# Performance work log

Hardware: AMD Instinct MI355X
Metric: run time of the kernel (lower is better)

Reference implementation:

```python
import jax, jax.numpy as jnp
import numpy as np
import math

H = 10  # hidden_dim (hardcoded in source)
D = 2   # data_dim (hardcoded in source)
T = 256
B = 2048

PARAM_SHAPES = {
    'fi_in_W': (D, H), 'fi_in_b': (H,), 'fi_h_W': (H, H), 'fi_h_b': (H,),
    'fi_mu_W': (H, H), 'fi_mu_b': (H,), 'fi_sg_W': (H, H), 'fi_sg_b': (H,),
    'inf_in_W': (D, H), 'inf_in_b': (H,), 'inf_j_W': (2 * H, H), 'inf_j_b': (H,),
    'inf_h_W': (H, H), 'inf_h_b': (H,), 'inf_mu_W': (H, H), 'inf_mu_b': (H,),
    'inf_sg_W': (H, H), 'inf_sg_b': (H,),
    'tr_h_W': (H, H), 'tr_h_b': (H,), 'tr_mu_W': (H, H), 'tr_mu_b': (H,),
    'tr_sg_W': (H, H), 'tr_sg_b': (H,),
    'gen_h1_W': (H, H), 'gen_h1_b': (H,), 'gen_h2_W': (H, H), 'gen_h2_b': (H,),
    'gen_mu_W': (H, D), 'gen_mu_b': (D,), 'gen_sg_W': (H, D), 'gen_sg_b': (D,),
}


def setup_inputs() -> dict:
    key = jax.random.key(0)
    names = list(PARAM_SHAPES)
    keys = jax.random.split(key, len(names) + 2)
    inp = {}
    inp['sequence'] = jax.random.normal(keys[0], (T, B, D), jnp.float32)
    inp['noise'] = jax.random.normal(keys[1], (T, B, H), jnp.float32)
    for n, k in zip(names, keys[2:]):
        inp[n] = 0.1 * jax.random.normal(k, PARAM_SHAPES[n], jnp.float32)
    # Transition sigma is tanh(.); shift its bias so sigma stays strictly positive
    # (a trained model would do the same; negative sigma makes the source's log(prod) NaN).
    inp['tr_sg_b'] = inp['tr_sg_b'] + 2.0
    return inp


def _forward(sequence, noise,
             fi_in_W, fi_in_b, fi_h_W, fi_h_b, fi_mu_W, fi_mu_b, fi_sg_W, fi_sg_b,
             inf_in_W, inf_in_b, inf_j_W, inf_j_b, inf_h_W, inf_h_b, inf_mu_W, inf_mu_b, inf_sg_W, inf_sg_b,
             tr_h_W, tr_h_b, tr_mu_W, tr_mu_b, tr_sg_W, tr_sg_b,
             gen_h1_W, gen_h1_b, gen_h2_W, gen_h2_b, gen_mu_W, gen_mu_b, gen_sg_W, gen_sg_b):

    def first_inf(x):
        h = jnp.tanh(x @ fi_in_W + fi_in_b)
        h = jnp.tanh(h @ fi_h_W + fi_h_b)
        return jnp.tanh(h @ fi_mu_W + fi_mu_b), jax.nn.sigmoid(h @ fi_sg_W + fi_sg_b) + 0.001

    def inference(x, z):
        e = jnp.tanh(x @ inf_in_W + inf_in_b)
        h = jnp.tanh(jnp.concatenate([e, z], -1) @ inf_j_W + inf_j_b)
        h = jnp.tanh(h @ inf_h_W + inf_h_b)
        return jnp.tanh(h @ inf_mu_W + inf_mu_b), jax.nn.sigmoid(h @ inf_sg_W + inf_sg_b) + 0.001

    def transition(z):
        h = jnp.tanh(z @ tr_h_W + tr_h_b)
        return jnp.tanh(h @ tr_mu_W + tr_mu_b), jnp.tanh(h @ tr_sg_W + tr_sg_b)

    def generator(z):
        h = jax.nn.relu(z @ gen_h1_W + gen_h1_b)
        h = jax.nn.relu(h @ gen_h2_W + gen_h2_b)
        return jax.nn.sigmoid(h @ gen_mu_W + gen_mu_b), jax.nn.sigmoid(h @ gen_sg_W + gen_sg_b)

    def kld(mu_q, sg_q, mu_p, sg_p):  # source GaussianKLD (treats sigma as variance)
        a = jnp.log(jnp.prod(sg_p, -1) / jnp.prod(sg_q, -1))
        b = jnp.sum(sg_q / sg_p, -1)
        c = jnp.sum((mu_p - mu_q) ** 2 / sg_p, -1)
        return 0.5 * (a + b + c - mu_q.shape[-1])

    def gll(mu, sg, target):  # source GaussianLL (note: log(pi), not 2*pi — faithful)
        a = jnp.log(jnp.prod(sg, -1))
        b = jnp.sum((target - mu) ** 2 / sg, -1)
        c = mu.shape[-1] * math.log(math.pi)
        return -0.5 * (a + b + c)

    # t = 0: first_inference against unit-Gaussian prior
    q_mu0, q_sg0 = first_inf(sequence[0])
    kl0 = kld(q_mu0, q_sg0, jnp.zeros_like(q_mu0), jnp.ones_like(q_sg0))
    z1 = q_mu0 + q_sg0 * noise[0]
    g_mu0, g_sg0 = generator(z1)
    loss0 = kl0 + gll(g_mu0, g_sg0, sequence[0])  # [B]

    def step(z_prev, xe):
        x_t, eps = xe
        pr_mu, pr_sg = transition(z_prev)
        q_mu, q_sg = inference(x_t, z_prev)
        kl_t = kld(q_mu, q_sg, pr_mu, pr_sg)
        z = q_mu + q_sg * eps
        m, s = generator(z)
        ll_t = gll(m, s, x_t)
        return z, (m, kl_t + ll_t)

    _, (gens_rest, step_losses) = jax.lax.scan(step, z1, (sequence[1:], noise[1:]))
    generations = jnp.concatenate([g_mu0[None], gens_rest], 0)  # [T, B, D]
    loss = loss0 + jnp.sum(step_losses, 0)                       # [B]
    return generations, -loss / sequence.shape[0]


def reference(sequence, noise,
              fi_in_W, fi_in_b, fi_h_W, fi_h_b, fi_mu_W, fi_mu_b, fi_sg_W, fi_sg_b,
              inf_in_W, inf_in_b, inf_j_W, inf_j_b, inf_h_W, inf_h_b, inf_mu_W, inf_mu_b, inf_sg_W, inf_sg_b,
              tr_h_W, tr_h_b, tr_mu_W, tr_mu_b, tr_sg_W, tr_sg_b,
              gen_h1_W, gen_h1_b, gen_h2_W, gen_h2_b, gen_mu_W, gen_mu_b, gen_sg_W, gen_sg_b):
    return _forward(sequence, noise,
                    fi_in_W, fi_in_b, fi_h_W, fi_h_b, fi_mu_W, fi_mu_b, fi_sg_W, fi_sg_b,
                    inf_in_W, inf_in_b, inf_j_W, inf_j_b, inf_h_W, inf_h_b, inf_mu_W, inf_mu_b, inf_sg_W, inf_sg_b,
                    tr_h_W, tr_h_b, tr_mu_W, tr_mu_b, tr_sg_W, tr_sg_b,
                    gen_h1_W, gen_h1_b, gen_h2_W, gen_h2_b, gen_mu_W, gen_mu_b, gen_sg_W, gen_sg_b)
```

## Files before the change

### kernel.cpp

```cpp
#include <hip/hip_runtime.h>
#include <math.h>

#define T_STEPS 256
#define BATCH   2048
#define HID     10

#define S2P  2.8853900817779268f
#define SNP -1.4426950408889634f
#define LN2  0.6931471805599453f
#define LOGPI 1.1447298858494002f

typedef float v2f __attribute__((ext_vector_type(2)));

__device__ __forceinline__ float frcp(float x){ return __builtin_amdgcn_rcpf(x); }
__device__ __forceinline__ float ex2 (float x){ return __builtin_amdgcn_exp2f(x); }
__device__ __forceinline__ float ftanh2(float y){ return 1.f - 2.f*frcp(1.f + ex2(y)); }
__device__ __forceinline__ float fsigm2(float y){ return frcp(1.f + ex2(y)); }

template<int K> __device__ __forceinline__ float rotk(float x){
  return __int_as_float(__builtin_amdgcn_update_dpp(
      0, __float_as_int(x), 0x120 + K, 0xF, 0xF, false));
}
#define ROT16(r, v) do{ float _v=(v); r[0]=_v; \
  r[1]=rotk<1>(_v);  r[2]=rotk<2>(_v);  r[3]=rotk<3>(_v);  r[4]=rotk<4>(_v);  \
  r[5]=rotk<5>(_v);  r[6]=rotk<6>(_v);  r[7]=rotk<7>(_v);  r[8]=rotk<8>(_v);  \
  r[9]=rotk<9>(_v);  r[10]=rotk<10>(_v);r[11]=rotk<11>(_v);r[12]=rotk<12>(_v);\
  r[13]=rotk<13>(_v);r[14]=rotk<14>(_v);r[15]=rotk<15>(_v); }while(0)

__device__ __forceinline__ float dot16(const float* r, const float* w, float bias){
  float a0 = fmaf(r[0], w[0], bias);
  float a1 = r[1]*w[1];
  float a2 = r[2]*w[2];
  float a3 = r[3]*w[3];
  #pragma unroll
  for (int k=4;k<16;k+=4){
    a0 = fmaf(r[k  ], w[k  ], a0);
    a1 = fmaf(r[k+1], w[k+1], a1);
    a2 = fmaf(r[k+2], w[k+2], a2);
    a3 = fmaf(r[k+3], w[k+3], a3);
  }
  return (a0+a1)+(a2+a3);
}
__device__ __forceinline__ v2f dotp16s(const float* r, const v2f* w, v2f init){
  v2f a0 = __builtin_elementwise_fma((v2f){r[0],r[0]}, w[0], init);
  v2f a1 = (v2f){r[1],r[1]}*w[1];
  v2f a2 = (v2f){r[2],r[2]}*w[2];
  v2f a3 = (v2f){r[3],r[3]}*w[3];
  #pragma unroll
  for (int k=4;k<16;k+=4){
    a0 = __builtin_elementwise_fma((v2f){r[k  ],r[k  ]}, w[k  ], a0);
    a1 = __builtin_elementwise_fma((v2f){r[k+1],r[k+1]}, w[k+1], a1);
    a2 = __builtin_elementwise_fma((v2f){r[k+2],r[k+2]}, w[k+2], a2);
    a3 = __builtin_elementwise_fma((v2f){r[k+3],r[k+3]}, w[k+3], a3);
  }
  return (a0+a1)+(a2+a3);
}

template<int NROW, int NCOL>
__device__ __forceinline__ void loadrot(float* dst, const float* W, int j, int col,
                                        bool colok, float scale){
  int colc = colok ? col : 0;
  #pragma unroll
  for (int k=0;k<16;k++){
    int i = (j - k) & 15;
    bool v = colok && (i < NROW);
    int ic = v ? i : 0;
    float w = W[ic*NCOL + colc];
    dst[k] = v ? scale*w : 0.f;
  }
}
__device__ __forceinline__ float bload(const float* p, int idx, bool ok, float scale){
  float t = p[ok ? idx : 0];
  return ok ? scale*t : 0.f;
}
template<int X> __device__ __forceinline__ float xor16(float x){
  return __int_as_float(__builtin_amdgcn_ds_swizzle(__float_as_int(x), (X<<10)|0x1f));
}

struct P34 { const float* p[34]; float* out; };

__global__ __attribute__((amdgpu_flat_work_group_size(128, 128), amdgpu_waves_per_eu(1, 1)))
void k_fused(P34 prm)
{
  __shared__ float s_ae[2][64];
  __shared__ float s_z [2][64];
  __shared__ float s_t0[4];

  const int tx   = threadIdx.x;
  const int wid  = tx >> 6;
  const int lane = tx & 63;
  const int j    = lane & 15;
  const int grp  = lane >> 4;
  const int b    = blockIdx.x*4 + grp;
  const bool act = (j < HID);
  const int  jl  = act ? j : 0;

  const float* __restrict__ seq   = prm.p[0];
  const float* __restrict__ noise = prm.p[1];
  float* __restrict__ out = prm.out;

  if (wid == 0){
    float w_jz[16]; loadrot<10,10>(w_jz, prm.p[12] + 100, j, j, act, S2P);
    float w_h [16]; loadrot<10,10>(w_h,  prm.p[14],       j, j, act, S2P);
    float tmu [16]; loadrot<10,10>(tmu,  prm.p[16],       j, j, act, S2P);
    float tsg [16]; loadrot<10,10>(tsg,  prm.p[18],       j, j, act, SNP);
    v2f wmsg[16];
    #pragma unroll
    for (int k=0;k<16;k++) wmsg[k] = (v2f){tmu[k], tsg[k]};
    float b_in_h  = bload(prm.p[15], jl, act, S2P);
    const v2f bmsg = (v2f){bload(prm.p[17], jl, act, S2P), bload(prm.p[19], jl, act, SNP)};
    float wth [16]; loadrot<10,10>(wth,  prm.p[20], j, j, act, S2P);
    float bth  = bload(prm.p[21], jl, act, S2P);
    float ttmu[16]; loadrot<10,10>(ttmu, prm.p[22], j, j, act, S2P);
    float ttsg[16]; loadrot<10,10>(ttsg, prm.p[24], j, j, act, S2P);
    v2f wpr[16];
    #pragma unroll
    for (int k=0;k<16;k++) wpr[k] = (v2f){ttmu[k], ttsg[k]};
    const v2f bpr = (v2f){bload(prm.p[23], jl, act, S2P), bload(prm.p[25], jl, act, S2P)};

    float LL = 0.f, L2 = 0.f;
    auto lde = [&](int t){ return noise[t*BATCH*HID + b*HID + jl]; };

    float z_prev;
    {
      float w0 = bload(prm.p[2],      jl, act, S2P);
      float w1 = bload(prm.p[2], 10 + jl, act, S2P);
      float bb = bload(prm.p[3], jl, act, S2P);
      float f_h[16], f_mu[16], f_sg[16];
      loadrot<10,10>(f_h,  prm.p[4], j, j, act, S2P);  float fb_h  = bload(prm.p[5], jl, act, S2P);
      loadrot<10,10>(f_mu, prm.p[6], j, j, act, S2P);  float fb_mu = bload(prm.p[7], jl, act, S2P);
      loadrot<10,10>(f_sg, prm.p[8], j, j, act, SNP);  float fb_sg = bload(prm.p[9], jl, act, SNP);
      float2 x0 = *reinterpret_cast<const float2*>(seq + b*2);
      float eps = lde(0);
      float h0 = ftanh2(fmaf(x0.x, w0, fmaf(x0.y, w1, bb)));
      float r0[16]; ROT16(r0, h0);
      float h1 = ftanh2(dot16(r0, f_h, fb_h));
      float r1[16]; ROT16(r1, h1);
      float mu = ftanh2(dot16(r1, f_mu, fb_mu));
      float sg = fsigm2(dot16(r1, f_sg, fb_sg)) + 0.001f;
      if (act){ LL += sg + mu*mu; L2 -= __log2f(sg); }
      z_prev = fmaf(sg, eps, mu);
      s_z[0][lane] = z_prev;
    }
    float e0=lde(1), e1=lde(2), e2=lde(3), e3=lde(4);
    __syncthreads();

    auto w0step = [&](const float* aeb, float* zb, float ec){
      float aev = aeb[lane];
      float rz[16]; ROT16(rz, z_prev);
      float hj = ftanh2(aev + dot16(rz, w_jz, 0.f));
      float rhj[16]; ROT16(rhj, hj);
      float hi = ftanh2(dot16(rhj, w_h, b_in_h));
      float rhi[16]; ROT16(rhi, hi);
      v2f d2 = dotp16s(rhi, wmsg, bmsg);
      float q_mu = ftanh2(d2.x);
      float q_sg = fsigm2(d2.y) + 0.001f;
      float z = fmaf(q_sg, ec, q_mu);
      zb[lane] = z;
      float th = ftanh2(dot16(rz, wth, bth));
      float rth[16]; ROT16(rth, th);
      v2f d3 = dotp16s(rth, wpr, bpr);
      float prmu = ftanh2(d3.x);
      float prsg = ftanh2(d3.y);
      if (act){
        float dmu = prmu - q_mu;
        float rp  = frcp(prsg);
        LL += (q_sg + dmu*dmu)*rp;
        L2 += __log2f(prsg) - __log2f(q_sg);
      }
      z_prev = z;
    };

    for (int p = 0; p < 125; ++p){
      int s = 2*p + 1;
      float n0 = lde(s+4), n1 = lde(s+5);
      w0step(s_ae[1], s_z[1], e0); __syncthreads();
      w0step(s_ae[0], s_z[0], e1); __syncthreads();
      e0=e2; e1=e3; e2=n0; e3=n1;
    }
    float e255 = lde(255);
    w0step(s_ae[1], s_z[1], e0);   __syncthreads();
    w0step(s_ae[0], s_z[0], e1);   __syncthreads();
    w0step(s_ae[1], s_z[1], e2);   __syncthreads();
    w0step(s_ae[0], s_z[0], e3);   __syncthreads();
    w0step(s_ae[1], s_z[1], e255); __syncthreads();

    float tot = fmaf(LN2, L2, LL);
    tot += xor16<1>(tot); tot += xor16<2>(tot); tot += xor16<4>(tot); tot += xor16<8>(tot);
    if (j == 0) s_t0[grp] = tot;
    __syncthreads();
  } else {
    float w_ii0   = bload(prm.p[10],      jl, act, S2P);
    float w_ii1   = bload(prm.p[10], 10 + jl, act, S2P);
    float b_in_in = bload(prm.p[11], jl, act, S2P);
    float w_je[16]; loadrot<10,10>(w_je, prm.p[12], j, j, act, S2P);
    float b_in_j  = bload(prm.p[13], jl, act, S2P);

    float wg1[16]; loadrot<10,10>(wg1, prm.p[26], j, j, act, 1.f);
    float bg1 = bload(prm.p[27], jl, act, 1.f);
    float wg2[16]; loadrot<10,10>(wg2, prm.p[28], j, j, act, 1.f);
    float bg2 = bload(prm.p[29], jl, act, 1.f);
    const bool isd = (j < 4);
    const float* Wgo = (j < 2) ? prm.p[30] : prm.p[32];
    const float* Bgo = (j < 2) ? prm.p[31] : prm.p[33];
    float wgo[16]; loadrot<10,2>(wgo, Wgo, j, j & 1, isd, SNP);
    float bgo = bload(Bgo, j & 1, isd, SNP);

    float LL = 0.f, L2 = 0.f;
    auto ldx = [&](int t){ return *reinterpret_cast<const float2*>(seq + t*BATCH*2 + b*2); };

    {
      float2 x1 = ldx(1);
      float e = ftanh2(fmaf(x1.x, w_ii0, fmaf(x1.y, w_ii1, b_in_in)));
      float re[16]; ROT16(re, e);
      s_ae[1][lane] = dot16(re, w_je, b_in_j);
    }
    float2 xA = ldx(0), xB = ldx(1), xC = ldx(2), xD = ldx(3);
    __syncthreads();

    auto w1step = [&](const float* zb, float* aeb, float2 xgll, float2 xe, int tG, bool do_e){
      float zl = zb[lane];
      if (do_e){
        float e = ftanh2(fmaf(xe.x, w_ii0, fmaf(xe.y, w_ii1, b_in_in)));
        float re[16]; ROT16(re, e);
        aeb[lane] = dot16(re, w_je, b_in_j);
      }
      float rz[16]; ROT16(rz, zl);
      float g1 = fmaxf(dot16(rz, wg1, bg1), 0.f);
      float rg1[16]; ROT16(rg1, g1);
      float g2 = fmaxf(dot16(rg1, wg2, bg2), 0.f);
      float rg2[16]; ROT16(rg2, g2);
      float ygo = dot16(rg2, wgo, bgo);
      float tgo = 1.f + ex2(ygo);
      float tpl = rotk<14>(tgo);
      if (j < 2){
        float m = frcp(tgo);
        out[tG*(BATCH*2) + b*2 + j] = m;
        float dd = ((j==0) ? xgll.x : xgll.y) - m;
        LL -= dd*dd*tpl;
        L2 += __log2f(tpl);
      }
    };

    for (int p = 0; p < 125; ++p){
      int s = 2*p + 1;
      float2 n0 = ldx(s+3), n1 = ldx(s+4);
      w1step(s_z[0], s_ae[0], xA, xC, s-1, true); __syncthreads();
      w1step(s_z[1], s_ae[1], xB, xD, s,   true); __syncthreads();
      xA=xC; xB=xD; xC=n0; xD=n1;
    }
    float2 x254 = ldx(254), x255 = ldx(255);
    w1step(s_z[0], s_ae[0], xA, xC,   250, true);  __syncthreads();
    w1step(s_z[1], s_ae[1], xB, xD,   251, true);  __syncthreads();
    w1step(s_z[0], s_ae[0], xC, x254, 252, true);  __syncthreads();
    w1step(s_z[1], s_ae[1], xD, x255, 253, true);  __syncthreads();
    w1step(s_z[0], s_ae[0], x254, x255, 254, false); __syncthreads();
    w1step(s_z[1], s_ae[1], x255, x255, 255, false);

    float tot = fmaf(LN2, L2, LL);
    tot += xor16<1>(tot); tot += xor16<2>(tot); tot += xor16<4>(tot); tot += xor16<8>(tot);
    __syncthreads();
    if (j == 0)
      out[T_STEPS*BATCH*2 + b] = -(tot + s_t0[grp])*(1.0f/512.0f) + 5.0f + LOGPI;
  }
}

extern "C" void kernel_launch(void* const* d_in, const int* in_sizes, int n_in,
                              void* d_out, int out_size, void* d_ws, size_t ws_size,
                              hipStream_t stream) {
  P34 prm;
  for (int i = 0; i < 34; ++i) prm.p[i] = (const float*)d_in[i];
  prm.out = (float*)d_out;
  hipLaunchKernelGGL(k_fused, dim3(512), dim3(128), 0, stream, prm);
}
```

Measured before the change: 143.6 us.

## Split recurrence into three-wave pipeline moving transition/KL work off critical wave

The block grows from two to three waves. Wave 0 now runs only the inference recurrence (z chain), wave 1 computes the encoder embedding one step ahead plus the transition prior and KL term one step behind, and wave 2 runs the generator and likelihood. The transition MLP no longer sits on the serial dependency chain of wave 0, which should shorten each step's critical path. In exchange there are more LDS buffers (a 4-deep z ring and q_mu/q_sg staging), an extra wave per block, and a per-step barrier across three waves; the packed v2f dot products are replaced by scalar dots.

```diff
diff --git a/kernel.cpp b/kernel.cpp
--- a/kernel.cpp
+++ b/kernel.cpp
@@ -9,8 +9,6 @@
 #define SNP -1.4426950408889634f
 #define LN2  0.6931471805599453f
 #define LOGPI 1.1447298858494002f
-
-typedef float v2f __attribute__((ext_vector_type(2)));
 
 __device__ __forceinline__ float frcp(float x){ return __builtin_amdgcn_rcpf(x); }
 __device__ __forceinline__ float ex2 (float x){ return __builtin_amdgcn_exp2f(x); }
@@ -41,20 +39,6 @@
   }
   return (a0+a1)+(a2+a3);
 }
-__device__ __forceinline__ v2f dotp16s(const float* r, const v2f* w, v2f init){
-  v2f a0 = __builtin_elementwise_fma((v2f){r[0],r[0]}, w[0], init);
-  v2f a1 = (v2f){r[1],r[1]}*w[1];
-  v2f a2 = (v2f){r[2],r[2]}*w[2];
-  v2f a3 = (v2f){r[3],r[3]}*w[3];
-  #pragma unroll
-  for (int k=4;k<16;k+=4){
-    a0 = __builtin_elementwise_fma((v2f){r[k  ],r[k  ]}, w[k  ], a0);
-    a1 = __builtin_elementwise_fma((v2f){r[k+1],r[k+1]}, w[k+1], a1);
-    a2 = __builtin_elementwise_fma((v2f){r[k+2],r[k+2]}, w[k+2], a2);
-    a3 = __builtin_elementwise_fma((v2f){r[k+3],r[k+3]}, w[k+3], a3);
-  }
-  return (a0+a1)+(a2+a3);
-}
 
 template<int NROW, int NCOL>
 __device__ __forceinline__ void loadrot(float* dst, const float* W, int j, int col,
@@ -79,15 +63,17 @@
 
 struct P34 { const float* p[34]; float* out; };
 
-__global__ __attribute__((amdgpu_flat_work_group_size(128, 128), amdgpu_waves_per_eu(1, 1)))
+__global__ __attribute__((amdgpu_flat_work_group_size(192, 192), amdgpu_waves_per_eu(1, 1)))
 void k_fused(P34 prm)
 {
-  __shared__ float s_ae[2][64];
-  __shared__ float s_z [2][64];
-  __shared__ float s_t0[4];
+  __shared__ float zb [4][64];
+  __shared__ float qmB[2][64];
+  __shared__ float qsB[2][64];
+  __shared__ float aeB[2][64];
+  __shared__ float part[3][4];
 
   const int tx   = threadIdx.x;
-  const int wid  = tx >> 6;
+  const int wid  = tx / 64;
   const int lane = tx & 63;
   const int j    = lane & 15;
   const int grp  = lane >> 4;
@@ -99,26 +85,17 @@
   const float* __restrict__ noise = prm.p[1];
   float* __restrict__ out = prm.out;
 
+  float LL = 0.f, L2 = 0.f;
+
   if (wid == 0){
     float w_jz[16]; loadrot<10,10>(w_jz, prm.p[12] + 100, j, j, act, S2P);
     float w_h [16]; loadrot<10,10>(w_h,  prm.p[14],       j, j, act, S2P);
-    float tmu [16]; loadrot<10,10>(tmu,  prm.p[16],       j, j, act, S2P);
-    float tsg [16]; loadrot<10,10>(tsg,  prm.p[18],       j, j, act, SNP);
-    v2f wmsg[16];
-    #pragma unroll
-    for (int k=0;k<16;k++) wmsg[k] = (v2f){tmu[k], tsg[k]};
+    float wmu [16]; loadrot<10,10>(wmu,  prm.p[16],       j, j, act, S2P);
+    float wsg [16]; loadrot<10,10>(wsg,  prm.p[18],       j, j, act, SNP);
     float b_in_h  = bload(prm.p[15], jl, act, S2P);
-    const v2f bmsg = (v2f){bload(prm.p[17], jl, act, S2P), bload(prm.p[19], jl, act, SNP)};
-    float wth [16]; loadrot<10,10>(wth,  prm.p[20], j, j, act, S2P);
-    float bth  = bload(prm.p[21], jl, act, S2P);
-    float ttmu[16]; loadrot<10,10>(ttmu, prm.p[22], j, j, act, S2P);
-    float ttsg[16]; loadrot<10,10>(ttsg, prm.p[24], j, j, act, S2P);
-    v2f wpr[16];
-    #pragma unroll
-    for (int k=0;k<16;k++) wpr[k] = (v2f){ttmu[k], ttsg[k]};
-    const v2f bpr = (v2f){bload(prm.p[23], jl, act, S2P), bload(prm.p[25], jl, act, S2P)};
-
-    float LL = 0.f, L2 = 0.f;
+    float b_mu    = bload(prm.p[17], jl, act, S2P);
+    float b_sg    = bload(prm.p[19], jl, act, SNP);
+
     auto lde = [&](int t){ return noise[t*BATCH*HID + b*HID + jl]; };
 
     float z_prev;
@@ -140,62 +117,85 @@
       float sg = fsigm2(dot16(r1, f_sg, fb_sg)) + 0.001f;
       if (act){ LL += sg + mu*mu; L2 -= __log2f(sg); }
       z_prev = fmaf(sg, eps, mu);
-      s_z[0][lane] = z_prev;
+      zb[0][lane] = z_prev;
     }
     float e0=lde(1), e1=lde(2), e2=lde(3), e3=lde(4);
     __syncthreads();
 
-    auto w0step = [&](const float* aeb, float* zb, float ec){
-      float aev = aeb[lane];
-      float rz[16]; ROT16(rz, z_prev);
-      float hj = ftanh2(aev + dot16(rz, w_jz, 0.f));
-      float rhj[16]; ROT16(rhj, hj);
-      float hi = ftanh2(dot16(rhj, w_h, b_in_h));
-      float rhi[16]; ROT16(rhi, hi);
-      v2f d2 = dotp16s(rhi, wmsg, bmsg);
-      float q_mu = ftanh2(d2.x);
-      float q_sg = fsigm2(d2.y) + 0.001f;
-      float z = fmaf(q_sg, ec, q_mu);
-      zb[lane] = z;
-      float th = ftanh2(dot16(rz, wth, bth));
-      float rth[16]; ROT16(rth, th);
-      v2f d3 = dotp16s(rth, wpr, bpr);
-      float prmu = ftanh2(d3.x);
-      float prsg = ftanh2(d3.y);
-      if (act){
-        float dmu = prmu - q_mu;
-        float rp  = frcp(prsg);
-        LL += (q_sg + dmu*dmu)*rp;
-        L2 += __log2f(prsg) - __log2f(q_sg);
-      }
-      z_prev = z;
-    };
-
-    for (int p = 0; p < 125; ++p){
-      int s = 2*p + 1;
-      float n0 = lde(s+4), n1 = lde(s+5);
-      w0step(s_ae[1], s_z[1], e0); __syncthreads();
-      w0step(s_ae[0], s_z[0], e1); __syncthreads();
-      e0=e2; e1=e3; e2=n0; e3=n1;
-    }
-    float e255 = lde(255);
-    w0step(s_ae[1], s_z[1], e0);   __syncthreads();
-    w0step(s_ae[0], s_z[0], e1);   __syncthreads();
-    w0step(s_ae[1], s_z[1], e2);   __syncthreads();
-    w0step(s_ae[0], s_z[0], e3);   __syncthreads();
-    w0step(s_ae[1], s_z[1], e255); __syncthreads();
-
-    float tot = fmaf(LN2, L2, LL);
-    tot += xor16<1>(tot); tot += xor16<2>(tot); tot += xor16<4>(tot); tot += xor16<8>(tot);
-    if (j == 0) s_t0[grp] = tot;
-    __syncthreads();
-  } else {
+    for (int s = 1; s <= 256; ++s){
+      if (s <= 255){
+        int tn = s + 4; if (tn > 255) tn = 255;
+        float en = lde(tn);
+        float aev = aeB[s&1][lane];
+        float rz[16]; ROT16(rz, z_prev);
+        float hj = ftanh2(aev + dot16(rz, w_jz, 0.f));
+        float rhj[16]; ROT16(rhj, hj);
+        float hi = ftanh2(dot16(rhj, w_h, b_in_h));
+        float rhi[16]; ROT16(rhi, hi);
+        float q_mu = ftanh2(dot16(rhi, wmu, b_mu));
+        float q_sg = fsigm2(dot16(rhi, wsg, b_sg)) + 0.001f;
+        float z = fmaf(q_sg, e0, q_mu);
+        zb [s&3][lane] = z;
+        qmB[s&1][lane] = q_mu;
+        qsB[s&1][lane] = q_sg;
+        z_prev = z;
+        e0=e1; e1=e2; e2=e3; e3=en;
+      }
+      __syncthreads();
+    }
+  } else if (wid == 1){
     float w_ii0   = bload(prm.p[10],      jl, act, S2P);
     float w_ii1   = bload(prm.p[10], 10 + jl, act, S2P);
     float b_in_in = bload(prm.p[11], jl, act, S2P);
     float w_je[16]; loadrot<10,10>(w_je, prm.p[12], j, j, act, S2P);
     float b_in_j  = bload(prm.p[13], jl, act, S2P);
 
+    float wth [16]; loadrot<10,10>(wth,  prm.p[20], j, j, act, S2P);
+    float bth  = bload(prm.p[21], jl, act, S2P);
+    float wtmu[16]; loadrot<10,10>(wtmu, prm.p[22], j, j, act, S2P);
+    float btmu = bload(prm.p[23], jl, act, S2P);
+    float wtsg[16]; loadrot<10,10>(wtsg, prm.p[24], j, j, act, S2P);
+    float btsg = bload(prm.p[25], jl, act, S2P);
+
+    auto ldx = [&](int t){ return *reinterpret_cast<const float2*>(seq + t*BATCH*2 + b*2); };
+
+    {
+      float2 x1 = ldx(1);
+      float e = ftanh2(fmaf(x1.x, w_ii0, fmaf(x1.y, w_ii1, b_in_in)));
+      float re[16]; ROT16(re, e);
+      aeB[1][lane] = dot16(re, w_je, b_in_j);
+    }
+    float2 xq0 = ldx(2), xq1 = ldx(3);
+    __syncthreads();
+
+    for (int s = 1; s <= 256; ++s){
+      if (s <= 254){
+        int tn = s + 3; if (tn > 255) tn = 255;
+        float2 xn = ldx(tn);
+        float e = ftanh2(fmaf(xq0.x, w_ii0, fmaf(xq0.y, w_ii1, b_in_in)));
+        float re[16]; ROT16(re, e);
+        aeB[(s+1)&1][lane] = dot16(re, w_je, b_in_j);
+        xq0 = xq1; xq1 = xn;
+      }
+      if (s >= 2){
+        float zp  = zb [(s-2)&3][lane];
+        float qmu = qmB[(s-1)&1][lane];
+        float qsg = qsB[(s-1)&1][lane];
+        float rz[16]; ROT16(rz, zp);
+        float th = ftanh2(dot16(rz, wth, bth));
+        float rth[16]; ROT16(rth, th);
+        float prmu = ftanh2(dot16(rth, wtmu, btmu));
+        float prsg = ftanh2(dot16(rth, wtsg, btsg));
+        if (act){
+          float dmu = prmu - qmu;
+          float rp  = frcp(prsg);
+          LL += (qsg + dmu*dmu)*rp;
+          L2 += __log2f(prsg) - __log2f(qsg);
+        }
+      }
+      __syncthreads();
+    }
+  } else {
     float wg1[16]; loadrot<10,10>(wg1, prm.p[26], j, j, act, 1.f);
     float bg1 = bload(prm.p[27], jl, act, 1.f);
     float wg2[16]; loadrot<10,10>(wg2, prm.p[28], j, j, act, 1.f);
@@ -206,25 +206,14 @@
     float wgo[16]; loadrot<10,2>(wgo, Wgo, j, j & 1, isd, SNP);
     float bgo = bload(Bgo, j & 1, isd, SNP);
 
-    float LL = 0.f, L2 = 0.f;
     auto ldx = [&](int t){ return *reinterpret_cast<const float2*>(seq + t*BATCH*2 + b*2); };
-
-    {
-      float2 x1 = ldx(1);
-      float e = ftanh2(fmaf(x1.x, w_ii0, fmaf(x1.y, w_ii1, b_in_in)));
-      float re[16]; ROT16(re, e);
-      s_ae[1][lane] = dot16(re, w_je, b_in_j);
-    }
-    float2 xA = ldx(0), xB = ldx(1), xC = ldx(2), xD = ldx(3);
+    float2 xg = ldx(0), xg1 = ldx(1);
     __syncthreads();
 
-    auto w1step = [&](const float* zb, float* aeb, float2 xgll, float2 xe, int tG, bool do_e){
-      float zl = zb[lane];
-      if (do_e){
-        float e = ftanh2(fmaf(xe.x, w_ii0, fmaf(xe.y, w_ii1, b_in_in)));
-        float re[16]; ROT16(re, e);
-        aeb[lane] = dot16(re, w_je, b_in_j);
-      }
+    for (int s = 1; s <= 256; ++s){
+      int tn = s + 1; if (tn > 255) tn = 255;
+      float2 xn = ldx(tn);
+      float zl = zb[(s-1)&3][lane];
       float rz[16]; ROT16(rz, zl);
       float g1 = fmaxf(dot16(rz, wg1, bg1), 0.f);
       float rg1[16]; ROT16(rg1, g1);
@@ -235,34 +224,23 @@
       float tpl = rotk<14>(tgo);
       if (j < 2){
         float m = frcp(tgo);
-        out[tG*(BATCH*2) + b*2 + j] = m;
-        float dd = ((j==0) ? xgll.x : xgll.y) - m;
+        out[(s-1)*(BATCH*2) + b*2 + j] = m;
+        float dd = ((j==0) ? xg.x : xg.y) - m;
         LL -= dd*dd*tpl;
         L2 += __log2f(tpl);
       }
-    };
-
-    for (int p = 0; p < 125; ++p){
-      int s = 2*p + 1;
-      float2 n0 = ldx(s+3), n1 = ldx(s+4);
-      w1step(s_z[0], s_ae[0], xA, xC, s-1, true); __syncthreads();
-      w1step(s_z[1], s_ae[1], xB, xD, s,   true); __syncthreads();
-      xA=xC; xB=xD; xC=n0; xD=n1;
-    }
-    float2 x254 = ldx(254), x255 = ldx(255);
-    w1step(s_z[0], s_ae[0], xA, xC,   250, true);  __syncthreads();
-    w1step(s_z[1], s_ae[1], xB, xD,   251, true);  __syncthreads();
-    w1step(s_z[0], s_ae[0], xC, x254, 252, true);  __syncthreads();
-    w1step(s_z[1], s_ae[1], xD, x255, 253, true);  __syncthreads();
-    w1step(s_z[0], s_ae[0], x254, x255, 254, false); __syncthreads();
-    w1step(s_z[1], s_ae[1], x255, x255, 255, false);
-
-    float tot = fmaf(LN2, L2, LL);
-    tot += xor16<1>(tot); tot += xor16<2>(tot); tot += xor16<4>(tot); tot += xor16<8>(tot);
-    __syncthreads();
-    if (j == 0)
-      out[T_STEPS*BATCH*2 + b] = -(tot + s_t0[grp])*(1.0f/512.0f) + 5.0f + LOGPI;
+      xg = xg1; xg1 = xn;
+      __syncthreads();
+    }
   }
+
+  float tot = fmaf(LN2, L2, LL);
+  tot += xor16<1>(tot); tot += xor16<2>(tot); tot += xor16<4>(tot); tot += xor16<8>(tot);
+  if (j == 0) part[wid][grp] = tot;
+  __syncthreads();
+  if (wid == 0 && j == 0)
+    out[T_STEPS*BATCH*2 + b] =
+      -(part[0][grp] + part[1][grp] + part[2][grp])*(1.0f/512.0f) + 5.0f + LOGPI;
 }
 
 extern "C" void kernel_launch(void* const* d_in, const int* in_sizes, int n_in,
@@ -271,5 +249,5 @@
   P34 prm;
   for (int i = 0; i < 34; ++i) prm.p[i] = (const float*)d_in[i];
   prm.out = (float*)d_out;
-  hipLaunchKernelGGL(k_fused, dim3(512), dim3(128), 0, stream, prm);
-}
+  hipLaunchKernelGGL(k_fused, dim3(512), dim3(192), 0, stream, prm);
+}
```

After: 257.9 us. +79.6%, slower.

## Halve block barriers by processing two timesteps per sync with 4-slot LDS ring

Applied to the files above, without the earlier changes.

Moves from one __syncthreads per timestep to one per pair of timesteps by enlarging the shared ring buffers for the encoded-input and latent values from 2 to 4 slots. The producer wave runs two recurrent steps per barrier while the consumer wave computes encodings two steps ahead and the generator/loss for the two previous steps. The aim is to cut barrier stalls on the serial recurrence, at the cost of a deeper producer/consumer skew, more LDS, and boundary guards in the loop. The final loss reduction is also unified to after both branches.

```diff
diff --git a/kernel.cpp b/kernel.cpp
--- a/kernel.cpp
+++ b/kernel.cpp
@@ -76,15 +76,16 @@
 template<int X> __device__ __forceinline__ float xor16(float x){
   return __int_as_float(__builtin_amdgcn_ds_swizzle(__float_as_int(x), (X<<10)|0x1f));
 }
+__device__ __forceinline__ int imin255(int t){ return t > 255 ? 255 : t; }
 
 struct P34 { const float* p[34]; float* out; };
 
 __global__ __attribute__((amdgpu_flat_work_group_size(128, 128), amdgpu_waves_per_eu(1, 1)))
 void k_fused(P34 prm)
 {
-  __shared__ float s_ae[2][64];
-  __shared__ float s_z [2][64];
-  __shared__ float s_t0[4];
+  __shared__ float s_ae[4][64];
+  __shared__ float s_z [4][64];
+  __shared__ float part[2][4];
 
   const int tx   = threadIdx.x;
   const int wid  = tx >> 6;
@@ -98,6 +99,8 @@
   const float* __restrict__ seq   = prm.p[0];
   const float* __restrict__ noise = prm.p[1];
   float* __restrict__ out = prm.out;
+
+  float LL = 0.f, L2 = 0.f;
 
   if (wid == 0){
     float w_jz[16]; loadrot<10,10>(w_jz, prm.p[12] + 100, j, j, act, S2P);
@@ -118,7 +121,6 @@
     for (int k=0;k<16;k++) wpr[k] = (v2f){ttmu[k], ttsg[k]};
     const v2f bpr = (v2f){bload(prm.p[23], jl, act, S2P), bload(prm.p[25], jl, act, S2P)};
 
-    float LL = 0.f, L2 = 0.f;
     auto lde = [&](int t){ return noise[t*BATCH*HID + b*HID + jl]; };
 
     float z_prev;
@@ -145,8 +147,8 @@
     float e0=lde(1), e1=lde(2), e2=lde(3), e3=lde(4);
     __syncthreads();
 
-    auto w0step = [&](const float* aeb, float* zb, float ec){
-      float aev = aeb[lane];
+    auto w0step = [&](int sl, float ec){
+      float aev = s_ae[sl][lane];
       float rz[16]; ROT16(rz, z_prev);
       float hj = ftanh2(aev + dot16(rz, w_jz, 0.f));
       float rhj[16]; ROT16(rhj, hj);
@@ -156,7 +158,7 @@
       float q_mu = ftanh2(d2.x);
       float q_sg = fsigm2(d2.y) + 0.001f;
       float z = fmaf(q_sg, ec, q_mu);
-      zb[lane] = z;
+      s_z[sl][lane] = z;
       float th = ftanh2(dot16(rz, wth, bth));
       float rth[16]; ROT16(rth, th);
       v2f d3 = dotp16s(rth, wpr, bpr);
@@ -171,24 +173,15 @@
       z_prev = z;
     };
 
-    for (int p = 0; p < 125; ++p){
-      int s = 2*p + 1;
-      float n0 = lde(s+4), n1 = lde(s+5);
-      w0step(s_ae[1], s_z[1], e0); __syncthreads();
-      w0step(s_ae[0], s_z[0], e1); __syncthreads();
+    for (int k = 0; k < 128; ++k){
+      int s0 = 2*k + 1, s1 = s0 + 1;
+      float n0 = lde(imin255(s0+4)), n1 = lde(imin255(s0+5));
+      int sl0 = s0 & 3;
+      w0step(sl0, e0);
+      if (s1 <= 255) w0step((sl0+1)&3, e1);
       e0=e2; e1=e3; e2=n0; e3=n1;
+      __syncthreads();
     }
-    float e255 = lde(255);
-    w0step(s_ae[1], s_z[1], e0);   __syncthreads();
-    w0step(s_ae[0], s_z[0], e1);   __syncthreads();
-    w0step(s_ae[1], s_z[1], e2);   __syncthreads();
-    w0step(s_ae[0], s_z[0], e3);   __syncthreads();
-    w0step(s_ae[1], s_z[1], e255); __syncthreads();
-
-    float tot = fmaf(LN2, L2, LL);
-    tot += xor16<1>(tot); tot += xor16<2>(tot); tot += xor16<4>(tot); tot += xor16<8>(tot);
-    if (j == 0) s_t0[grp] = tot;
-    __syncthreads();
   } else {
     float w_ii0   = bload(prm.p[10],      jl, act, S2P);
     float w_ii1   = bload(prm.p[10], 10 + jl, act, S2P);
@@ -206,25 +199,15 @@
     float wgo[16]; loadrot<10,2>(wgo, Wgo, j, j & 1, isd, SNP);
     float bgo = bload(Bgo, j & 1, isd, SNP);
 
-    float LL = 0.f, L2 = 0.f;
     auto ldx = [&](int t){ return *reinterpret_cast<const float2*>(seq + t*BATCH*2 + b*2); };
 
-    {
-      float2 x1 = ldx(1);
-      float e = ftanh2(fmaf(x1.x, w_ii0, fmaf(x1.y, w_ii1, b_in_in)));
+    auto estage = [&](float2 xe, int sl){
+      float e = ftanh2(fmaf(xe.x, w_ii0, fmaf(xe.y, w_ii1, b_in_in)));
       float re[16]; ROT16(re, e);
-      s_ae[1][lane] = dot16(re, w_je, b_in_j);
-    }
-    float2 xA = ldx(0), xB = ldx(1), xC = ldx(2), xD = ldx(3);
-    __syncthreads();
-
-    auto w1step = [&](const float* zb, float* aeb, float2 xgll, float2 xe, int tG, bool do_e){
-      float zl = zb[lane];
-      if (do_e){
-        float e = ftanh2(fmaf(xe.x, w_ii0, fmaf(xe.y, w_ii1, b_in_in)));
-        float re[16]; ROT16(re, e);
-        aeb[lane] = dot16(re, w_je, b_in_j);
-      }
+      s_ae[sl][lane] = dot16(re, w_je, b_in_j);
+    };
+    auto genstep = [&](int sl, int tG, float2 xg){
+      float zl = s_z[sl][lane];
       float rz[16]; ROT16(rz, zl);
       float g1 = fmaxf(dot16(rz, wg1, bg1), 0.f);
       float rg1[16]; ROT16(rg1, g1);
@@ -236,33 +219,39 @@
       if (j < 2){
         float m = frcp(tgo);
         out[tG*(BATCH*2) + b*2 + j] = m;
-        float dd = ((j==0) ? xgll.x : xgll.y) - m;
+        float dd = ((j==0) ? xg.x : xg.y) - m;
         LL -= dd*dd*tpl;
         L2 += __log2f(tpl);
       }
     };
 
-    for (int p = 0; p < 125; ++p){
-      int s = 2*p + 1;
-      float2 n0 = ldx(s+3), n1 = ldx(s+4);
-      w1step(s_z[0], s_ae[0], xA, xC, s-1, true); __syncthreads();
-      w1step(s_z[1], s_ae[1], xB, xD, s,   true); __syncthreads();
-      xA=xC; xB=xD; xC=n0; xD=n1;
+    float2 x1 = ldx(1), x2 = ldx(2);
+    estage(x1, 1); estage(x2, 2);
+    float2 xB = ldx(0), xC = x1, xD = x2, xe0 = ldx(3), xe1 = ldx(4);
+    float2 xA = xB;
+    __syncthreads();
+
+    for (int k = 0; k < 128; ++k){
+      int t0 = 2*k + 3, t1 = t0 + 1;
+      float2 xen0 = ldx(imin255(t0+2)), xen1 = ldx(imin255(t0+3));
+      if (t0 <= 255) estage(xe0, t0 & 3);
+      if (t1 <= 255) estage(xe1, t1 & 3);
+      int tg = 2*k;
+      if (k >= 1) genstep((tg-1) & 3, tg-1, xA);
+      genstep(tg & 3, tg, xB);
+      xA=xC; xB=xD; xC=xe0; xD=xe1; xe0=xen0; xe1=xen1;
+      __syncthreads();
     }
-    float2 x254 = ldx(254), x255 = ldx(255);
-    w1step(s_z[0], s_ae[0], xA, xC,   250, true);  __syncthreads();
-    w1step(s_z[1], s_ae[1], xB, xD,   251, true);  __syncthreads();
-    w1step(s_z[0], s_ae[0], xC, x254, 252, true);  __syncthreads();
-    w1step(s_z[1], s_ae[1], xD, x255, 253, true);  __syncthreads();
-    w1step(s_z[0], s_ae[0], x254, x255, 254, false); __syncthreads();
-    w1step(s_z[1], s_ae[1], x255, x255, 255, false);
-
-    float tot = fmaf(LN2, L2, LL);
-    tot += xor16<1>(tot); tot += xor16<2>(tot); tot += xor16<4>(tot); tot += xor16<8>(tot);
-    __syncthreads();
-    if (j == 0)
-      out[T_STEPS*BATCH*2 + b] = -(tot + s_t0[grp])*(1.0f/512.0f) + 5.0f + LOGPI;
-  }
+    genstep(3, 255, xA);
+  }
+
+  float tot = fmaf(LN2, L2, LL);
+  tot += xor16<1>(tot); tot += xor16<2>(tot); tot += xor16<4>(tot); tot += xor16<8>(tot);
+  if (j == 0) part[wid][grp] = tot;
+  __syncthreads();
+  if (wid == 0 && j == 0)
+    out[T_STEPS*BATCH*2 + b] =
+      -(part[0][grp] + part[1][grp])*(1.0f/512.0f) + 5.0f + LOGPI;
 }
 
 extern "C" void kernel_launch(void* const* d_in, const int* in_sizes, int n_in,
```

After: 142.5 us (median of 2 runs). No clear change (-0.8%).
